# Kernel optimization log

Hardware: AMD Instinct MI355X
Metric: run time of the kernel (lower is better)

The kernel has to match this reference:

```python
import jax, jax.numpy as jnp
import numpy as np

D_MODEL = 2048
N_HEADS = 16
HEAD_DIM = D_MODEL // N_HEADS  # 128
FF_DIM = 512


def setup_inputs() -> dict:
    key = jax.random.key(0)
    k_x, k_w1, k_b1, k_w2, k_b2 = jax.random.split(key, 5)
    x = jax.random.normal(k_x, (4, 4096, D_MODEL), dtype=jnp.float32)
    # Per-head Linear params, stacked over heads. torch Linear init ~ U(-1/sqrt(fan_in), 1/sqrt(fan_in))
    lim1 = 1.0 / np.sqrt(HEAD_DIM)
    lim2 = 1.0 / np.sqrt(FF_DIM)
    W1 = jax.random.uniform(k_w1, (N_HEADS, HEAD_DIM, FF_DIM), jnp.float32, -lim1, lim1)
    b1 = jax.random.uniform(k_b1, (N_HEADS, FF_DIM), jnp.float32, -lim1, lim1)
    W2 = jax.random.uniform(k_w2, (N_HEADS, FF_DIM, HEAD_DIM), jnp.float32, -lim2, lim2)
    b2 = jax.random.uniform(k_b2, (N_HEADS, HEAD_DIM), jnp.float32, -lim2, lim2)
    return {"x": x, "W1": W1, "b1": b1, "W2": W2, "b2": b2}


def reference(x, W1, b1, W2, b2):
    bs, seq, _ = x.shape
    # [bs, seq, H, head_dim]
    xh = x.reshape(bs, seq, N_HEADS, HEAD_DIM)
    # fused per-head FFN as batched GEMMs (dropout is identity at eval / p used only in training)
    h = jnp.einsum('bshd,hdf->bshf', xh, W1) + b1  # [bs, seq, H, ff]
    h = jax.nn.relu(h)
    out = jnp.einsum('bshf,hfd->bshd', h, W2) + b2  # [bs, seq, H, head_dim]
    return out.reshape(bs, seq, D_MODEL)
```

## Files before the change

### kernel.cpp

```cpp
#include <hip/hip_runtime.h>


typedef __attribute__((ext_vector_type(8))) short short8;
typedef __attribute__((ext_vector_type(4))) short short4v;
typedef __attribute__((ext_vector_type(4))) float f32x4;

#define NHEADS 16
#define DHEAD  128
#define NFF    512
#define DMODEL 2048
#define NTOK   16384
#define MT     128
#define FC     128
#define CH_SH  16384

__device__ __forceinline__ short f2bf(float f) {
    unsigned u = __builtin_bit_cast(unsigned, f);
    u += 0x7FFFu + ((u >> 16) & 1u);
    return (short)(u >> 16);
}

#define GLDS16(g, l) __builtin_amdgcn_global_load_lds( \
    (__attribute__((address_space(1))) void*)(g), \
    (__attribute__((address_space(3))) void*)(l), 16, 0, 0)

__global__ __launch_bounds__(256) void transpose_both(
        const float* __restrict__ W1, const float* __restrict__ W2,
        short* __restrict__ w1x, short* __restrict__ w2x) {
    __shared__ float tile[64][65];
    const int z = blockIdx.z;
    const int which = z & 1, h = z >> 1;
    const int C = which ? DHEAD : NFF;
    const float* s = (which ? W2 : W1) + (size_t)h * DHEAD * NFF;
    short* dst = (which ? w2x : w1x) + (size_t)h * 4 * CH_SH;
    const int ct = C / 64;
    const int t0 = blockIdx.x;
    const int r0 = (t0 / ct) * 64, c0 = (t0 % ct) * 64;
    const int t = threadIdx.x;
    #pragma unroll
    for (int p = 0; p < 4; ++p) {
        int idx = p * 256 + t;
        int row = idx >> 4, col = (idx & 15) * 4;
        *(f32x4*)&tile[row][col] = *(const f32x4*)&s[(size_t)(r0 + row) * C + c0 + col];
    }
    __syncthreads();
    #pragma unroll
    for (int it = 0; it < 2; ++it) {
        int u = it * 256 + t;
        int dr = u >> 3, g = u & 7;
        short8 v;
        #pragma unroll
        for (int j = 0; j < 8; ++j) v[j] = f2bf(tile[g * 8 + j][dr]);
        size_t idx;
        if (which == 0) {
            int f = c0 + dr;
            int gd = (r0 >> 3) + g;
            idx = (size_t)(f >> 7) * CH_SH + (size_t)(f & 127) * 128 + ((gd ^ (f & 7)) << 3);
        } else {
            int d = c0 + dr;
            int gf = ((r0 & 127) >> 3) + g;
            idx = (size_t)(r0 >> 7) * CH_SH + (size_t)d * 128 + ((gf ^ (d & 7)) << 3);
        }
        *(short8*)&dst[idx] = v;
    }
}

__global__ __launch_bounds__(512, 2) void ffn_main(
        const float* __restrict__ x,
        const short* __restrict__ w1x,
        const float* __restrict__ b1,
        const short* __restrict__ w2x,
        const float* __restrict__ b2,
        float* __restrict__ out) {
    __shared__ short W1s[2][CH_SH];
    __shared__ short W2s[CH_SH];
    __shared__ short Hs[CH_SH];
    __shared__ float Bs[NFF];

    const int m0   = blockIdx.x * MT;
    const int h    = blockIdx.y;
    const int tid  = threadIdx.x;
    const int lane = tid & 63;
    const int wave = tid >> 6;
    const int quad = lane >> 4;
    const int l16  = lane & 15;
    const int wf   = wave >> 2;
    const int wm   = wave & 3;
    const int s7   = l16 & 7;

    Bs[tid] = b1[h * NFF + tid];

    {
        const char* src = (const char*)(w1x + (size_t)h * 4 * CH_SH);
        char* dl = (char*)&W1s[0][0];
        #pragma unroll
        for (int i = 0; i < 4; ++i)
            GLDS16(src + wave * 4096 + i * 1024 + lane * 16, dl + wave * 4096 + i * 1024);
    }

    short8 xf[2][4];
    {
        const float* xb = x + (size_t)(m0 + wm * 32) * DMODEL + h * DHEAD;
        #pragma unroll
        for (int mi = 0; mi < 2; ++mi)
            #pragma unroll
            for (int kk = 0; kk < 4; ++kk) {
                const float* p = xb + (size_t)(mi * 16 + l16) * DMODEL + kk * 32 + quad * 8;
                f32x4 a = *(const f32x4*)(p);
                f32x4 b = *(const f32x4*)(p + 4);
                short8 v;
                v[0] = f2bf(a[0]); v[1] = f2bf(a[1]); v[2] = f2bf(a[2]); v[3] = f2bf(a[3]);
                v[4] = f2bf(b[0]); v[5] = f2bf(b[1]); v[6] = f2bf(b[2]); v[7] = f2bf(b[3]);
                xf[mi][kk] = v;
            }
    }

    f32x4 acc2[4][2];
    #pragma unroll
    for (int di = 0; di < 4; ++di)
        #pragma unroll
        for (int mi = 0; mi < 2; ++mi)
            acc2[di][mi] = (f32x4){0.f, 0.f, 0.f, 0.f};

    const int arow = wf * 64 + l16;

    #pragma unroll
    for (int c = 0; c < 4; ++c) {
        {
            const char* src = (const char*)(w2x + ((size_t)h * 4 + c) * CH_SH);
            char* dl = (char*)W2s;
            #pragma unroll
            for (int i = 0; i < 4; ++i)
                GLDS16(src + wave * 4096 + i * 1024 + lane * 16, dl + wave * 4096 + i * 1024);
        }
        if (c < 3) {
            const char* src = (const char*)(w1x + ((size_t)h * 4 + c + 1) * CH_SH);
            char* dl = (char*)&W1s[(c + 1) & 1][0];
            #pragma unroll
            for (int i = 0; i < 4; ++i)
                GLDS16(src + wave * 4096 + i * 1024 + lane * 16, dl + wave * 4096 + i * 1024);
        }
        if (c < 3) asm volatile("s_waitcnt vmcnt(8) lgkmcnt(0)" ::: "memory");
        else       asm volatile("s_waitcnt vmcnt(4) lgkmcnt(0)" ::: "memory");
        __builtin_amdgcn_s_barrier();

        f32x4 acc1[4][2];
        #pragma unroll
        for (int fi = 0; fi < 4; ++fi)
            #pragma unroll
            for (int mi = 0; mi < 2; ++mi)
                acc1[fi][mi] = (f32x4){0.f, 0.f, 0.f, 0.f};
        #pragma unroll
        for (int kk = 0; kk < 4; ++kk) {
            short8 af[4];
            #pragma unroll
            for (int fi = 0; fi < 4; ++fi)
                af[fi] = *(const short8*)&W1s[c & 1][(size_t)(arow + fi * 16) * 128 +
                                                    ((((kk << 2) + quad) ^ s7) << 3)];
            #pragma unroll
            for (int fi = 0; fi < 4; ++fi)
                #pragma unroll
                for (int mi = 0; mi < 2; ++mi)
                    acc1[fi][mi] = __builtin_amdgcn_mfma_f32_16x16x32_bf16(
                        af[fi], xf[mi][kk], acc1[fi][mi], 0, 0, 0);
        }

        #pragma unroll
        for (int fi = 0; fi < 4; ++fi) {
            f32x4 bb = *(const f32x4*)&Bs[c * FC + wf * 64 + fi * 16 + quad * 4];
            #pragma unroll
            for (int mi = 0; mi < 2; ++mi) {
                int mr = wm * 32 + mi * 16 + l16;
                short4v hv;
                #pragma unroll
                for (int r = 0; r < 4; ++r)
                    hv[r] = f2bf(fmaxf(acc1[fi][mi][r] + bb[r], 0.f));
                int g = (wf * 8 + fi * 2 + (quad >> 1)) ^ s7;
                *(short4v*)&Hs[(size_t)mr * 128 + g * 8 + (quad & 1) * 4] = hv;
            }
        }
        if (c < 3) asm volatile("s_waitcnt vmcnt(4) lgkmcnt(0)" ::: "memory");
        else       asm volatile("s_waitcnt vmcnt(0) lgkmcnt(0)" ::: "memory");
        __builtin_amdgcn_s_barrier();

        #pragma unroll
        for (int kk = 0; kk < 4; ++kk) {
            short8 wfr[4], hfr[2];
            #pragma unroll
            for (int di = 0; di < 4; ++di)
                wfr[di] = *(const short8*)&W2s[(size_t)(arow + di * 16) * 128 +
                                              ((((kk << 2) + quad) ^ s7) << 3)];
            #pragma unroll
            for (int mi = 0; mi < 2; ++mi)
                hfr[mi] = *(const short8*)&Hs[(size_t)(wm * 32 + mi * 16 + l16) * 128 +
                                             ((((kk << 2) + quad) ^ s7) << 3)];
            #pragma unroll
            for (int di = 0; di < 4; ++di)
                #pragma unroll
                for (int mi = 0; mi < 2; ++mi)
                    acc2[di][mi] = __builtin_amdgcn_mfma_f32_16x16x32_bf16(
                        wfr[di], hfr[mi], acc2[di][mi], 0, 0, 0);
        }
        __builtin_amdgcn_s_barrier();
    }

    #pragma unroll
    for (int di = 0; di < 4; ++di) {
        f32x4 bb = *(const f32x4*)(b2 + h * DHEAD + wf * 64 + di * 16 + quad * 4);
        #pragma unroll
        for (int mi = 0; mi < 2; ++mi) {
            int m = m0 + wm * 32 + mi * 16 + l16;
            f32x4 ov;
            #pragma unroll
            for (int r = 0; r < 4; ++r)
                ov[r] = acc2[di][mi][r] + bb[r];
            *(f32x4*)(out + (size_t)m * DMODEL + h * DHEAD + wf * 64 + di * 16 + quad * 4) = ov;
        }
    }
}

extern "C" void kernel_launch(void* const* d_in, const int* in_sizes, int n_in,
                              void* d_out, int out_size, void* d_ws, size_t ws_size,
                              hipStream_t stream) {
    const float* x  = (const float*)d_in[0];
    const float* W1 = (const float*)d_in[1];
    const float* b1 = (const float*)d_in[2];
    const float* W2 = (const float*)d_in[3];
    const float* b2 = (const float*)d_in[4];
    float* out = (float*)d_out;

    short* w1x = (short*)d_ws;
    short* w2x = (short*)d_ws + (size_t)NHEADS * 4 * CH_SH;

    transpose_both<<<dim3(16, 1, 2 * NHEADS), 256, 0, stream>>>(W1, W2, w1x, w2x);
    ffn_main<<<dim3(NTOK / MT, NHEADS), 512, 0, stream>>>(x, w1x, b1, w2x, b2, out);
}
```

Baseline: 359.0 us.

## Make blocks persistent over 8 token tiles, keeping all of W1 resident in LDS

Each block now handles 8 token tiles for one head and loads the whole per-head W1 (128 KB) into LDS once, so weight staging is no longer repeated for every 128-row tile. W2 is stored in a plain transposed layout and its fragments are read straight from global memory into registers on each chunk, relying on L2/L1 instead of LDS. The b1 bias is also read from global memory rather than staged in LDS. The grid shrinks to 16x16 = 256 blocks and LDS use rises to about 160 KB, which cuts occupancy to one block per CU. Per-chunk global loads of W2 and x now sit directly in the compute loop with no prefetch to hide them.

Measured after the change: 450.7 us. +25.5%, slower.

```diff
diff --git a/kernel.cpp b/kernel.cpp
--- a/kernel.cpp
+++ b/kernel.cpp
@@ -11,6 +11,7 @@
 #define DMODEL 2048
 #define NTOK   16384
 #define MT     128
+#define MTILES 8
 #define FC     128
 #define CH_SH  16384
 
@@ -26,13 +27,13 @@
 
 __global__ __launch_bounds__(256) void transpose_both(
         const float* __restrict__ W1, const float* __restrict__ W2,
-        short* __restrict__ w1x, short* __restrict__ w2x) {
+        short* __restrict__ w1x, short* __restrict__ w2t) {
     __shared__ float tile[64][65];
     const int z = blockIdx.z;
     const int which = z & 1, h = z >> 1;
     const int C = which ? DHEAD : NFF;
     const float* s = (which ? W2 : W1) + (size_t)h * DHEAD * NFF;
-    short* dst = (which ? w2x : w1x) + (size_t)h * 4 * CH_SH;
+    short* dst = (which ? w2t : w1x) + (size_t)h * 4 * CH_SH;
     const int ct = C / 64;
     const int t0 = blockIdx.x;
     const int r0 = (t0 / ct) * 64, c0 = (t0 % ct) * 64;
@@ -51,17 +52,17 @@
         short8 v;
         #pragma unroll
         for (int j = 0; j < 8; ++j) v[j] = f2bf(tile[g * 8 + j][dr]);
-        size_t idx;
         if (which == 0) {
             int f = c0 + dr;
             int gd = (r0 >> 3) + g;
-            idx = (size_t)(f >> 7) * CH_SH + (size_t)(f & 127) * 128 + ((gd ^ (f & 7)) << 3);
+            size_t idx = (size_t)(f >> 7) * CH_SH + (size_t)(f & 127) * 128 +
+                         ((gd ^ (f & 7)) << 3);
+            *(short8*)&dst[idx] = v;
         } else {
             int d = c0 + dr;
-            int gf = ((r0 & 127) >> 3) + g;
-            idx = (size_t)(r0 >> 7) * CH_SH + (size_t)d * 128 + ((gf ^ (d & 7)) << 3);
-        }
-        *(short8*)&dst[idx] = v;
+            size_t idx = (size_t)d * NFF + r0 + g * 8;
+            *(short8*)&dst[idx] = v;
+        }
     }
 }
 
@@ -69,16 +70,14 @@
         const float* __restrict__ x,
         const short* __restrict__ w1x,
         const float* __restrict__ b1,
-        const short* __restrict__ w2x,
+        const short* __restrict__ w2t,
         const float* __restrict__ b2,
         float* __restrict__ out) {
-    __shared__ short W1s[2][CH_SH];
-    __shared__ short W2s[CH_SH];
+    __shared__ short W1s[4 * CH_SH];
     __shared__ short Hs[CH_SH];
-    __shared__ float Bs[NFF];
-
-    const int m0   = blockIdx.x * MT;
-    const int h    = blockIdx.y;
+
+    const int h      = blockIdx.y;
+    const int m_base = blockIdx.x * (MT * MTILES);
     const int tid  = threadIdx.x;
     const int lane = tid & 63;
     const int wave = tid >> 6;
@@ -88,133 +87,132 @@
     const int wm   = wave & 3;
     const int s7   = l16 & 7;
 
-    Bs[tid] = b1[h * NFF + tid];
-
     {
         const char* src = (const char*)(w1x + (size_t)h * 4 * CH_SH);
-        char* dl = (char*)&W1s[0][0];
-        #pragma unroll
-        for (int i = 0; i < 4; ++i)
-            GLDS16(src + wave * 4096 + i * 1024 + lane * 16, dl + wave * 4096 + i * 1024);
-    }
-
-    short8 xf[2][4];
-    {
-        const float* xb = x + (size_t)(m0 + wm * 32) * DMODEL + h * DHEAD;
-        #pragma unroll
-        for (int mi = 0; mi < 2; ++mi)
-            #pragma unroll
-            for (int kk = 0; kk < 4; ++kk) {
-                const float* p = xb + (size_t)(mi * 16 + l16) * DMODEL + kk * 32 + quad * 8;
-                f32x4 a = *(const f32x4*)(p);
-                f32x4 b = *(const f32x4*)(p + 4);
-                short8 v;
-                v[0] = f2bf(a[0]); v[1] = f2bf(a[1]); v[2] = f2bf(a[2]); v[3] = f2bf(a[3]);
-                v[4] = f2bf(b[0]); v[5] = f2bf(b[1]); v[6] = f2bf(b[2]); v[7] = f2bf(b[3]);
-                xf[mi][kk] = v;
-            }
-    }
-
-    f32x4 acc2[4][2];
+        char* dl = (char*)W1s;
+        #pragma unroll
+        for (int i = 0; i < 16; ++i)
+            GLDS16(src + (wave * 16 + i) * 1024 + lane * 16,
+                   dl + (wave * 16 + i) * 1024);
+    }
+
+    f32x4 bb2[4];
     #pragma unroll
     for (int di = 0; di < 4; ++di)
-        #pragma unroll
-        for (int mi = 0; mi < 2; ++mi)
-            acc2[di][mi] = (f32x4){0.f, 0.f, 0.f, 0.f};
+        bb2[di] = *(const f32x4*)(b2 + h * DHEAD + wf * 64 + di * 16 + quad * 4);
 
     const int arow = wf * 64 + l16;
-
-    #pragma unroll
-    for (int c = 0; c < 4; ++c) {
+    const short* w2b = w2t + (size_t)h * DHEAD * NFF + (size_t)(wf * 64 + l16) * NFF + quad * 8;
+
+    asm volatile("s_waitcnt vmcnt(0)" ::: "memory");
+    __builtin_amdgcn_s_barrier();
+
+    for (int mt = 0; mt < MTILES; ++mt) {
+        const int m0 = m_base + mt * MT;
+
+        short8 xf[2][4];
         {
-            const char* src = (const char*)(w2x + ((size_t)h * 4 + c) * CH_SH);
-            char* dl = (char*)W2s;
-            #pragma unroll
-            for (int i = 0; i < 4; ++i)
-                GLDS16(src + wave * 4096 + i * 1024 + lane * 16, dl + wave * 4096 + i * 1024);
-        }
-        if (c < 3) {
-            const char* src = (const char*)(w1x + ((size_t)h * 4 + c + 1) * CH_SH);
-            char* dl = (char*)&W1s[(c + 1) & 1][0];
-            #pragma unroll
-            for (int i = 0; i < 4; ++i)
-                GLDS16(src + wave * 4096 + i * 1024 + lane * 16, dl + wave * 4096 + i * 1024);
-        }
-        if (c < 3) asm volatile("s_waitcnt vmcnt(8) lgkmcnt(0)" ::: "memory");
-        else       asm volatile("s_waitcnt vmcnt(4) lgkmcnt(0)" ::: "memory");
-        __builtin_amdgcn_s_barrier();
-
-        f32x4 acc1[4][2];
-        #pragma unroll
-        for (int fi = 0; fi < 4; ++fi)
+            const float* xb = x + (size_t)(m0 + wm * 32) * DMODEL + h * DHEAD;
             #pragma unroll
             for (int mi = 0; mi < 2; ++mi)
-                acc1[fi][mi] = (f32x4){0.f, 0.f, 0.f, 0.f};
-        #pragma unroll
-        for (int kk = 0; kk < 4; ++kk) {
-            short8 af[4];
+                #pragma unroll
+                for (int kk = 0; kk < 4; ++kk) {
+                    const float* p = xb + (size_t)(mi * 16 + l16) * DMODEL + kk * 32 + quad * 8;
+                    f32x4 a = *(const f32x4*)(p);
+                    f32x4 b = *(const f32x4*)(p + 4);
+                    short8 v;
+                    v[0] = f2bf(a[0]); v[1] = f2bf(a[1]); v[2] = f2bf(a[2]); v[3] = f2bf(a[3]);
+                    v[4] = f2bf(b[0]); v[5] = f2bf(b[1]); v[6] = f2bf(b[2]); v[7] = f2bf(b[3]);
+                    xf[mi][kk] = v;
+                }
+        }
+
+        f32x4 acc2[4][2];
+        #pragma unroll
+        for (int di = 0; di < 4; ++di)
+            #pragma unroll
+            for (int mi = 0; mi < 2; ++mi)
+                acc2[di][mi] = (f32x4){0.f, 0.f, 0.f, 0.f};
+
+        #pragma unroll
+        for (int c = 0; c < 4; ++c) {
+            short8 wfr[4][4];
+            #pragma unroll
+            for (int kk = 0; kk < 4; ++kk)
+                #pragma unroll
+                for (int di = 0; di < 4; ++di)
+                    wfr[kk][di] = *(const short8*)(w2b + (size_t)(di * 16) * NFF + c * FC + kk * 32);
+            f32x4 bb1[4];
             #pragma unroll
             for (int fi = 0; fi < 4; ++fi)
-                af[fi] = *(const short8*)&W1s[c & 1][(size_t)(arow + fi * 16) * 128 +
-                                                    ((((kk << 2) + quad) ^ s7) << 3)];
+                bb1[fi] = *(const f32x4*)(b1 + h * NFF + c * FC + wf * 64 + fi * 16 + quad * 4);
+
+            f32x4 acc1[4][2];
             #pragma unroll
             for (int fi = 0; fi < 4; ++fi)
                 #pragma unroll
                 for (int mi = 0; mi < 2; ++mi)
-                    acc1[fi][mi] = __builtin_amdgcn_mfma_f32_16x16x32_bf16(
-                        af[fi], xf[mi][kk], acc1[fi][mi], 0, 0, 0);
-        }
-
-        #pragma unroll
-        for (int fi = 0; fi < 4; ++fi) {
-            f32x4 bb = *(const f32x4*)&Bs[c * FC + wf * 64 + fi * 16 + quad * 4];
+                    acc1[fi][mi] = (f32x4){0.f, 0.f, 0.f, 0.f};
+            #pragma unroll
+            for (int kk = 0; kk < 4; ++kk) {
+                short8 af[4];
+                #pragma unroll
+                for (int fi = 0; fi < 4; ++fi)
+                    af[fi] = *(const short8*)&W1s[c * CH_SH + (arow + fi * 16) * 128 +
+                                                 ((((kk << 2) + quad) ^ s7) << 3)];
+                #pragma unroll
+                for (int fi = 0; fi < 4; ++fi)
+                    #pragma unroll
+                    for (int mi = 0; mi < 2; ++mi)
+                        acc1[fi][mi] = __builtin_amdgcn_mfma_f32_16x16x32_bf16(
+                            af[fi], xf[mi][kk], acc1[fi][mi], 0, 0, 0);
+            }
+
+            __builtin_amdgcn_s_barrier();
+
+            #pragma unroll
+            for (int fi = 0; fi < 4; ++fi) {
+                #pragma unroll
+                for (int mi = 0; mi < 2; ++mi) {
+                    int mr = wm * 32 + mi * 16 + l16;
+                    short4v hv;
+                    #pragma unroll
+                    for (int r = 0; r < 4; ++r)
+                        hv[r] = f2bf(fmaxf(acc1[fi][mi][r] + bb1[fi][r], 0.f));
+                    int g = (wf * 8 + fi * 2 + (quad >> 1)) ^ s7;
+                    *(short4v*)&Hs[(size_t)mr * 128 + g * 8 + (quad & 1) * 4] = hv;
+                }
+            }
+            asm volatile("s_waitcnt lgkmcnt(0)" ::: "memory");
+            __builtin_amdgcn_s_barrier();
+
+            #pragma unroll
+            for (int kk = 0; kk < 4; ++kk) {
+                short8 hfr[2];
+                #pragma unroll
+                for (int mi = 0; mi < 2; ++mi)
+                    hfr[mi] = *(const short8*)&Hs[(size_t)(wm * 32 + mi * 16 + l16) * 128 +
+                                                 ((((kk << 2) + quad) ^ s7) << 3)];
+                #pragma unroll
+                for (int di = 0; di < 4; ++di)
+                    #pragma unroll
+                    for (int mi = 0; mi < 2; ++mi)
+                        acc2[di][mi] = __builtin_amdgcn_mfma_f32_16x16x32_bf16(
+                            wfr[kk][di], hfr[mi], acc2[di][mi], 0, 0, 0);
+            }
+        }
+
+        #pragma unroll
+        for (int di = 0; di < 4; ++di) {
             #pragma unroll
             for (int mi = 0; mi < 2; ++mi) {
-                int mr = wm * 32 + mi * 16 + l16;
-                short4v hv;
+                int m = m0 + wm * 32 + mi * 16 + l16;
+                f32x4 ov;
                 #pragma unroll
                 for (int r = 0; r < 4; ++r)
-                    hv[r] = f2bf(fmaxf(acc1[fi][mi][r] + bb[r], 0.f));
-                int g = (wf * 8 + fi * 2 + (quad >> 1)) ^ s7;
-                *(short4v*)&Hs[(size_t)mr * 128 + g * 8 + (quad & 1) * 4] = hv;
-            }
-        }
-        if (c < 3) asm volatile("s_waitcnt vmcnt(4) lgkmcnt(0)" ::: "memory");
-        else       asm volatile("s_waitcnt vmcnt(0) lgkmcnt(0)" ::: "memory");
-        __builtin_amdgcn_s_barrier();
-
-        #pragma unroll
-        for (int kk = 0; kk < 4; ++kk) {
-            short8 wfr[4], hfr[2];
-            #pragma unroll
-            for (int di = 0; di < 4; ++di)
-                wfr[di] = *(const short8*)&W2s[(size_t)(arow + di * 16) * 128 +
-                                              ((((kk << 2) + quad) ^ s7) << 3)];
-            #pragma unroll
-            for (int mi = 0; mi < 2; ++mi)
-                hfr[mi] = *(const short8*)&Hs[(size_t)(wm * 32 + mi * 16 + l16) * 128 +
-                                             ((((kk << 2) + quad) ^ s7) << 3)];
-            #pragma unroll
-            for (int di = 0; di < 4; ++di)
-                #pragma unroll
-                for (int mi = 0; mi < 2; ++mi)
-                    acc2[di][mi] = __builtin_amdgcn_mfma_f32_16x16x32_bf16(
-                        wfr[di], hfr[mi], acc2[di][mi], 0, 0, 0);
-        }
-        __builtin_amdgcn_s_barrier();
-    }
-
-    #pragma unroll
-    for (int di = 0; di < 4; ++di) {
-        f32x4 bb = *(const f32x4*)(b2 + h * DHEAD + wf * 64 + di * 16 + quad * 4);
-        #pragma unroll
-        for (int mi = 0; mi < 2; ++mi) {
-            int m = m0 + wm * 32 + mi * 16 + l16;
-            f32x4 ov;
-            #pragma unroll
-            for (int r = 0; r < 4; ++r)
-                ov[r] = acc2[di][mi][r] + bb[r];
-            *(f32x4*)(out + (size_t)m * DMODEL + h * DHEAD + wf * 64 + di * 16 + quad * 4) = ov;
+                    ov[r] = acc2[di][mi][r] + bb2[di][r];
+                *(f32x4*)(out + (size_t)m * DMODEL + h * DHEAD + wf * 64 + di * 16 + quad * 4) = ov;
+            }
         }
     }
 }
@@ -230,8 +228,8 @@
     float* out = (float*)d_out;
 
     short* w1x = (short*)d_ws;
-    short* w2x = (short*)d_ws + (size_t)NHEADS * 4 * CH_SH;
-
-    transpose_both<<<dim3(16, 1, 2 * NHEADS), 256, 0, stream>>>(W1, W2, w1x, w2x);
-    ffn_main<<<dim3(NTOK / MT, NHEADS), 512, 0, stream>>>(x, w1x, b1, w2x, b2, out);
-}
+    short* w2t = (short*)d_ws + (size_t)NHEADS * 4 * CH_SH;
+
+    transpose_both<<<dim3(16, 1, 2 * NHEADS), 256, 0, stream>>>(W1, W2, w1x, w2t);
+    ffn_main<<<dim3(NTOK / (MT * MTILES), NHEADS), 512, 0, stream>>>(x, w1x, b1, w2t, b2, out);
+}
```

## Double-buffer W1 and W2 chunks, remap grid head-fastest, keep biases in registers

Applied to the files above, without the earlier changes.

Both weight chunks are now double-buffered in LDS and prefetched for the next chunk right after the hidden-layer barrier, overlapping with the second GEMM instead of stalling mid-chunk on W2. The grid is flattened with head as the fast index so neighbouring blocks read the same x rows, improving cache locality. Bias staging in LDS is replaced by direct register loads. The extra W2 buffer raises LDS use, which may reduce blocks resident per CU.

Measured after the change: 332.8 us. 1.08x faster.

```diff
diff --git a/kernel.cpp b/kernel.cpp
--- a/kernel.cpp
+++ b/kernel.cpp
@@ -73,12 +73,12 @@
         const float* __restrict__ b2,
         float* __restrict__ out) {
     __shared__ short W1s[2][CH_SH];
-    __shared__ short W2s[CH_SH];
+    __shared__ short W2s[2][CH_SH];
     __shared__ short Hs[CH_SH];
-    __shared__ float Bs[NFF];
-
-    const int m0   = blockIdx.x * MT;
-    const int h    = blockIdx.y;
+
+    const int id   = blockIdx.x;
+    const int h    = id & 15;
+    const int m0   = (id >> 4) * MT;
     const int tid  = threadIdx.x;
     const int lane = tid & 63;
     const int wave = tid >> 6;
@@ -88,14 +88,20 @@
     const int wm   = wave & 3;
     const int s7   = l16 & 7;
 
-    Bs[tid] = b1[h * NFF + tid];
+    const short* w1h = w1x + (size_t)h * 4 * CH_SH;
+    const short* w2h = w2x + (size_t)h * 4 * CH_SH;
 
     {
-        const char* src = (const char*)(w1x + (size_t)h * 4 * CH_SH);
-        char* dl = (char*)&W1s[0][0];
+        const char* s1 = (const char*)w1h;
+        const char* s2 = (const char*)w2h;
+        char* d1 = (char*)&W1s[0][0];
+        char* d2 = (char*)&W2s[0][0];
         #pragma unroll
         for (int i = 0; i < 4; ++i)
-            GLDS16(src + wave * 4096 + i * 1024 + lane * 16, dl + wave * 4096 + i * 1024);
+            GLDS16(s1 + wave * 4096 + i * 1024 + lane * 16, d1 + wave * 4096 + i * 1024);
+        #pragma unroll
+        for (int i = 0; i < 4; ++i)
+            GLDS16(s2 + wave * 4096 + i * 1024 + lane * 16, d2 + wave * 4096 + i * 1024);
     }
 
     short8 xf[2][4];
@@ -115,6 +121,11 @@
             }
     }
 
+    f32x4 bb2[4];
+    #pragma unroll
+    for (int di = 0; di < 4; ++di)
+        bb2[di] = *(const f32x4*)(b2 + h * DHEAD + wf * 64 + di * 16 + quad * 4);
+
     f32x4 acc2[4][2];
     #pragma unroll
     for (int di = 0; di < 4; ++di)
@@ -124,25 +135,21 @@
 
     const int arow = wf * 64 + l16;
 
+    asm volatile("s_waitcnt vmcnt(0)" ::: "memory");
+    __builtin_amdgcn_s_barrier();
+
     #pragma unroll
     for (int c = 0; c < 4; ++c) {
-        {
-            const char* src = (const char*)(w2x + ((size_t)h * 4 + c) * CH_SH);
-            char* dl = (char*)W2s;
-            #pragma unroll
-            for (int i = 0; i < 4; ++i)
-                GLDS16(src + wave * 4096 + i * 1024 + lane * 16, dl + wave * 4096 + i * 1024);
-        }
-        if (c < 3) {
-            const char* src = (const char*)(w1x + ((size_t)h * 4 + c + 1) * CH_SH);
-            char* dl = (char*)&W1s[(c + 1) & 1][0];
-            #pragma unroll
-            for (int i = 0; i < 4; ++i)
-                GLDS16(src + wave * 4096 + i * 1024 + lane * 16, dl + wave * 4096 + i * 1024);
-        }
-        if (c < 3) asm volatile("s_waitcnt vmcnt(8) lgkmcnt(0)" ::: "memory");
-        else       asm volatile("s_waitcnt vmcnt(4) lgkmcnt(0)" ::: "memory");
-        __builtin_amdgcn_s_barrier();
+        const int buf = c & 1;
+        if (c) {
+            asm volatile("s_waitcnt vmcnt(0)" ::: "memory");
+            __builtin_amdgcn_s_barrier();
+        }
+
+        f32x4 bb1[4];
+        #pragma unroll
+        for (int fi = 0; fi < 4; ++fi)
+            bb1[fi] = *(const f32x4*)(b1 + h * NFF + c * FC + wf * 64 + fi * 16 + quad * 4);
 
         f32x4 acc1[4][2];
         #pragma unroll
@@ -155,8 +162,8 @@
             short8 af[4];
             #pragma unroll
             for (int fi = 0; fi < 4; ++fi)
-                af[fi] = *(const short8*)&W1s[c & 1][(size_t)(arow + fi * 16) * 128 +
-                                                    ((((kk << 2) + quad) ^ s7) << 3)];
+                af[fi] = *(const short8*)&W1s[buf][(size_t)(arow + fi * 16) * 128 +
+                                                  ((((kk << 2) + quad) ^ s7) << 3)];
             #pragma unroll
             for (int fi = 0; fi < 4; ++fi)
                 #pragma unroll
@@ -167,29 +174,40 @@
 
         #pragma unroll
         for (int fi = 0; fi < 4; ++fi) {
-            f32x4 bb = *(const f32x4*)&Bs[c * FC + wf * 64 + fi * 16 + quad * 4];
             #pragma unroll
             for (int mi = 0; mi < 2; ++mi) {
                 int mr = wm * 32 + mi * 16 + l16;
                 short4v hv;
                 #pragma unroll
                 for (int r = 0; r < 4; ++r)
-                    hv[r] = f2bf(fmaxf(acc1[fi][mi][r] + bb[r], 0.f));
+                    hv[r] = f2bf(fmaxf(acc1[fi][mi][r] + bb1[fi][r], 0.f));
                 int g = (wf * 8 + fi * 2 + (quad >> 1)) ^ s7;
                 *(short4v*)&Hs[(size_t)mr * 128 + g * 8 + (quad & 1) * 4] = hv;
             }
         }
-        if (c < 3) asm volatile("s_waitcnt vmcnt(4) lgkmcnt(0)" ::: "memory");
-        else       asm volatile("s_waitcnt vmcnt(0) lgkmcnt(0)" ::: "memory");
+        asm volatile("s_waitcnt lgkmcnt(0)" ::: "memory");
         __builtin_amdgcn_s_barrier();
+
+        if (c < 3) {
+            const char* s1 = (const char*)(w1h + (size_t)(c + 1) * CH_SH);
+            const char* s2 = (const char*)(w2h + (size_t)(c + 1) * CH_SH);
+            char* d1 = (char*)&W1s[buf ^ 1][0];
+            char* d2 = (char*)&W2s[buf ^ 1][0];
+            #pragma unroll
+            for (int i = 0; i < 4; ++i)
+                GLDS16(s1 + wave * 4096 + i * 1024 + lane * 16, d1 + wave * 4096 + i * 1024);
+            #pragma unroll
+            for (int i = 0; i < 4; ++i)
+                GLDS16(s2 + wave * 4096 + i * 1024 + lane * 16, d2 + wave * 4096 + i * 1024);
+        }
 
         #pragma unroll
         for (int kk = 0; kk < 4; ++kk) {
             short8 wfr[4], hfr[2];
             #pragma unroll
             for (int di = 0; di < 4; ++di)
-                wfr[di] = *(const short8*)&W2s[(size_t)(arow + di * 16) * 128 +
-                                              ((((kk << 2) + quad) ^ s7) << 3)];
+                wfr[di] = *(const short8*)&W2s[buf][(size_t)(arow + di * 16) * 128 +
+                                                   ((((kk << 2) + quad) ^ s7) << 3)];
             #pragma unroll
             for (int mi = 0; mi < 2; ++mi)
                 hfr[mi] = *(const short8*)&Hs[(size_t)(wm * 32 + mi * 16 + l16) * 128 +
@@ -201,19 +219,17 @@
                     acc2[di][mi] = __builtin_amdgcn_mfma_f32_16x16x32_bf16(
                         wfr[di], hfr[mi], acc2[di][mi], 0, 0, 0);
         }
-        __builtin_amdgcn_s_barrier();
     }
 
     #pragma unroll
     for (int di = 0; di < 4; ++di) {
-        f32x4 bb = *(const f32x4*)(b2 + h * DHEAD + wf * 64 + di * 16 + quad * 4);
         #pragma unroll
         for (int mi = 0; mi < 2; ++mi) {
             int m = m0 + wm * 32 + mi * 16 + l16;
             f32x4 ov;
             #pragma unroll
             for (int r = 0; r < 4; ++r)
-                ov[r] = acc2[di][mi][r] + bb[r];
+                ov[r] = acc2[di][mi][r] + bb2[di][r];
             *(f32x4*)(out + (size_t)m * DMODEL + h * DHEAD + wf * 64 + di * 16 + quad * 4) = ov;
         }
     }
@@ -233,5 +249,5 @@
     short* w2x = (short*)d_ws + (size_t)NHEADS * 4 * CH_SH;
 
     transpose_both<<<dim3(16, 1, 2 * NHEADS), 256, 0, stream>>>(W1, W2, w1x, w2x);
-    ffn_main<<<dim3(NTOK / MT, NHEADS), 512, 0, stream>>>(x, w1x, b1, w2x, b2, out);
-}
+    ffn_main<<<dim3(NTOK / MT * NHEADS), 512, 0, stream>>>(x, w1x, b1, w2x, b2, out);
+}
```
